# Optimization experiments

Hardware: AMD Instinct MI355X
Metric: run time of the kernel (lower is better)

Reference implementation:

```python
import jax, jax.numpy as jnp
import numpy as np

DIM = 1024
DIM_HEAD = 64
HEADS = 16
INNER = DIM_HEAD * HEADS  # 1024
B, N1, N2 = 8, 4096, 256
EPS = 1e-5


def layer_norm(x, w, b):
    mu = jnp.mean(x, axis=-1, keepdims=True)
    var = jnp.var(x, axis=-1, keepdims=True)
    return (x - mu) * jax.lax.rsqrt(var + EPS) * w + b


def setup_inputs() -> dict:
    key = jax.random.key(0)
    ks = jax.random.split(key, 10)
    return {
        "x": jax.random.normal(ks[0], (B, N1, DIM), jnp.float32),
        "latents": jax.random.normal(ks[1], (B, N2, DIM), jnp.float32),
        "shift": jax.random.normal(ks[2], (B, DIM), jnp.float32),
        "scale": jax.random.normal(ks[3], (B, DIM), jnp.float32),
        "ln1_w": jnp.ones((DIM,), jnp.float32),
        "ln1_b": jnp.zeros((DIM,), jnp.float32),
        "ln2_w": jnp.ones((DIM,), jnp.float32),
        "ln2_b": jnp.zeros((DIM,), jnp.float32),
        "Wq": jax.random.normal(ks[4], (INNER, DIM), jnp.float32) * 0.02,
        "Wkv": jax.random.normal(ks[5], (2 * INNER, DIM), jnp.float32) * 0.02,
        "Wo": jax.random.normal(ks[6], (DIM, INNER), jnp.float32) * 0.02,
    }


def reference(x, latents, shift, scale, ln1_w, ln1_b, ln2_w, ln2_b, Wq, Wkv, Wo):
    x = layer_norm(x, ln1_w, ln1_b)                      # (b, n1, D)
    lat = layer_norm(latents, ln2_w, ln2_b)              # (b, n2, D)
    lat = lat * (1.0 + scale[:, None, :]) + shift[:, None, :]

    b, n2, _ = lat.shape
    q = jnp.einsum('bld,ed->ble', lat, Wq)               # (b, n2, inner)
    kv_in = jnp.concatenate((x, lat), axis=-2)           # (b, n1+n2, D)
    kv = jnp.einsum('bld,ed->ble', kv_in, Wkv)           # (b, n1+n2, 2*inner)
    k, v = jnp.split(kv, 2, axis=-1)

    def to_heads(t):
        bsz, L, _ = t.shape
        return t.reshape(bsz, L, HEADS, DIM_HEAD).transpose(0, 2, 1, 3)

    q, k, v = to_heads(q), to_heads(k), to_heads(v)      # (b, h, L, dh)
    attn_scale = 1.0 / np.sqrt(np.sqrt(DIM_HEAD)).astype(np.float32)
    logits = jnp.einsum('bhqd,bhkd->bhqk', q * attn_scale, k * attn_scale)
    w = jax.nn.softmax(logits.astype(jnp.float32), axis=-1).astype(logits.dtype)
    out = jnp.einsum('bhqk,bhkd->bhqd', w, v)            # (b, h, n2, dh)
    out = out.transpose(0, 2, 1, 3).reshape(b, n2, INNER)
    return jnp.einsum('ble,de->bld', out, Wo)            # (b, n2, D)
```

## Files before the change

kernel.cpp:

```cpp
#include <hip/hip_runtime.h>
#include <cstdint>
#include <cstddef>

#define B_SZ 8
#define N1 4096
#define N2 256
#define LTOT 4352
#define DIMD 1024
#define HEADS 16
#define DH 64
#define MKV (B_SZ * LTOT)
#define ATILE 64
#define AITERS (LTOT / ATILE)
#define G0_BLOCKS 4352
#define MT_PER_XCD 34

typedef _Float16 f16;
typedef f16 f16x4_t __attribute__((ext_vector_type(4)));
typedef f16 f16x8_t __attribute__((ext_vector_type(8)));
typedef float f32x4_t __attribute__((ext_vector_type(4)));

__device__ __forceinline__ void g2l16(const void* g, void* l) {
  __builtin_amdgcn_global_load_lds(
      (__attribute__((address_space(1))) void*)g,
      (__attribute__((address_space(3))) void*)l, 16, 0, 0);
}


__global__ __launch_bounds__(256) void prep_kernel(
    const float* __restrict__ x, const float* __restrict__ lat,
    const float* __restrict__ shift, const float* __restrict__ scale,
    const float* __restrict__ ln1w, const float* __restrict__ ln1b,
    const float* __restrict__ ln2w, const float* __restrict__ ln2b,
    const float* __restrict__ Wq, const float* __restrict__ Wkv,
    const float* __restrict__ Wo, f16* __restrict__ kv_in,
    f16* __restrict__ Wq16, f16* __restrict__ Wkv16, f16* __restrict__ Wo16) {
  const int bid = blockIdx.x;
  const int tid = threadIdx.x;
  if (bid >= MKV) {
    const int c = bid - MKV;
    const float* src;
    f16* dst;
    int off;
    if (c < 1024) { src = Wq; dst = Wq16; off = c; }
    else if (c < 3072) { src = Wkv; dst = Wkv16; off = c - 1024; }
    else { src = Wo; dst = Wo16; off = c - 3072; }
    const int i = off * 256 + tid;
    float4 v = ((const float4*)src)[i];
    f16x4_t o = {(f16)v.x, (f16)v.y, (f16)v.z, (f16)v.w};
    ((f16x4_t*)dst)[i] = o;
    return;
  }
  const int row = bid;
  const int b = row / LTOT;
  const int n = row - b * LTOT;
  const bool is_lat = (n >= N1);
  const float* src = is_lat ? (lat + (size_t)(b * N2 + (n - N1)) * DIMD)
                            : (x + (size_t)(b * N1 + n) * DIMD);
  float4 v = ((const float4*)src)[tid];
  float s = v.x + v.y + v.z + v.w;
  float s2 = v.x * v.x + v.y * v.y + v.z * v.z + v.w * v.w;
#pragma unroll
  for (int m = 1; m <= 32; m <<= 1) {
    s += __shfl_xor(s, m, 64);
    s2 += __shfl_xor(s2, m, 64);
  }
  __shared__ float red[8];
  const int wave = tid >> 6;
  if ((tid & 63) == 0) { red[wave * 2] = s; red[wave * 2 + 1] = s2; }
  __syncthreads();
  s = red[0] + red[2] + red[4] + red[6];
  s2 = red[1] + red[3] + red[5] + red[7];
  const float mean = s * (1.0f / DIMD);
  const float var = fmaxf(s2 * (1.0f / DIMD) - mean * mean, 0.0f);
  const float rstd = rsqrtf(var + 1e-5f);
  const float4 w4 = ((const float4*)(is_lat ? ln2w : ln1w))[tid];
  const float4 b4 = ((const float4*)(is_lat ? ln2b : ln1b))[tid];
  float y0 = (v.x - mean) * rstd * w4.x + b4.x;
  float y1 = (v.y - mean) * rstd * w4.y + b4.y;
  float y2 = (v.z - mean) * rstd * w4.z + b4.z;
  float y3 = (v.w - mean) * rstd * w4.w + b4.w;
  if (is_lat) {
    float4 sc = ((const float4*)(scale + (size_t)b * DIMD))[tid];
    float4 sh = ((const float4*)(shift + (size_t)b * DIMD))[tid];
    y0 = y0 * (1.0f + sc.x) + sh.x;
    y1 = y1 * (1.0f + sc.y) + sh.y;
    y2 = y2 * (1.0f + sc.z) + sh.z;
    y3 = y3 * (1.0f + sc.w) + sh.w;
  }
  f16x4_t o = {(f16)y0, (f16)y1, (f16)y2, (f16)y3};
  *(f16x4_t*)(kv_in + (size_t)row * DIMD + tid * 4) = o;
}

__global__ __launch_bounds__(256, 4) void gemm_pre(
    const f16* __restrict__ kv_in, const f16* __restrict__ Wkv16,
    const f16* __restrict__ Wq16, f16* __restrict__ kbuf,
    f16* __restrict__ vbuf, f16* __restrict__ qbuf) {
  const int id = blockIdx.x;
  const bool is_kv = (id < G0_BLOCKS);
  int mt, nt;
  const f16 *Abase, *Bbase;
  if (is_kv) {
    const int xcd = id & 7, l = id >> 3;
    mt = xcd * MT_PER_XCD + (l >> 4);
    nt = l & 15;
    Abase = kv_in + (size_t)mt * 128 * DIMD;
    Bbase = Wkv16 + (size_t)nt * 128 * DIMD;
  } else {
    const int id2 = id - G0_BLOCKS;
    mt = id2 >> 3;
    nt = id2 & 7;
    const int bb = mt >> 1;
    Abase = kv_in + ((size_t)(bb * LTOT + N1 + (mt & 1) * 128)) * DIMD;
    Bbase = Wq16 + (size_t)nt * 128 * DIMD;
  }
  __shared__ alignas(16) f16 As[2][128 * 32];
  __shared__ alignas(16) f16 Bs[2][128 * 32];
  const int tid = threadIdx.x;
  const int wave = tid >> 6, lane = tid & 63;
  const int wm = (wave & 1) * 64, wn = (wave >> 1) * 64;
  const int lrow = lane >> 2, lcol = (lane & 3) * 8;
  const int r16 = lane & 15, g8 = (lane >> 4) * 8, q4 = (lane >> 4) * 4;
  const int lcol_sw = (((lane & 3) ^ ((lrow >> 1) & 3)) * 8);
  const int g8sw = (((lane >> 4) ^ ((r16 >> 1) & 3)) * 8);
  (void)lcol; (void)g8;
  f32x4_t acc[4][4] = {};

  auto stage = [&](int k0, int buf) {
    g2l16(Abase + (size_t)(wave * 16 + lrow) * DIMD + k0 + lcol_sw, &As[buf][(wave * 16) * 32]);
    g2l16(Abase + (size_t)(64 + wave * 16 + lrow) * DIMD + k0 + lcol_sw, &As[buf][(64 + wave * 16) * 32]);
    g2l16(Bbase + (size_t)(wave * 16 + lrow) * DIMD + k0 + lcol_sw, &Bs[buf][(wave * 16) * 32]);
    g2l16(Bbase + (size_t)(64 + wave * 16 + lrow) * DIMD + k0 + lcol_sw, &Bs[buf][(64 + wave * 16) * 32]);
  };
  auto body = [&](int kt, int cur) {
    if (kt < 31) asm volatile("s_waitcnt vmcnt(4)" ::: "memory");
    else         asm volatile("s_waitcnt vmcnt(0)" ::: "memory");
    asm volatile("s_barrier" ::: "memory");
    f16x8_t a[4], bf[4];
#pragma unroll
    for (int i = 0; i < 4; i++)
      a[i] = *(const f16x8_t*)&As[cur][(wm + i * 16 + r16) * 32 + g8sw];
#pragma unroll
    for (int j = 0; j < 4; j++)
      bf[j] = *(const f16x8_t*)&Bs[cur][(wn + j * 16 + r16) * 32 + g8sw];
#pragma unroll
    for (int i = 0; i < 4; i++)
#pragma unroll
      for (int j = 0; j < 4; j++)
        acc[i][j] = __builtin_amdgcn_mfma_f32_16x16x32_f16(a[i], bf[j], acc[i][j], 0, 0, 0);
    asm volatile("s_waitcnt lgkmcnt(0)" ::: "memory");
    asm volatile("s_barrier" ::: "memory");
    if (kt + 2 < 32) stage((kt + 2) * 32, cur);
  };
  stage(0, 0);
  stage(32, 1);
#pragma unroll 1
  for (int kt = 0; kt < 32; kt += 2) { body(kt, 0); body(kt + 1, 1); }

  if (is_kv) {
    const int m0 = mt * 128;
    const int b = m0 / LTOT;
    const int n0 = m0 - b * LTOT;
    const int e0 = nt * 128;
    if (e0 < 1024) {
#pragma unroll
      for (int i = 0; i < 4; i++) {
        const int n_base = n0 + wm + i * 16 + q4;
#pragma unroll
        for (int j = 0; j < 4; j++) {
          const int e = e0 + wn + j * 16 + r16;
          const int h = e >> 6, d = e & 63;
          const size_t base = ((size_t)(b * HEADS + h) * LTOT);
#pragma unroll
          for (int r = 0; r < 4; r++)
            kbuf[(base + n_base + r) * DH + d] = (f16)acc[i][j][r];
        }
      }
    } else {
      const int e0v = e0 - 1024;
#pragma unroll
      for (int i = 0; i < 4; i++) {
        const int n_base = n0 + wm + i * 16 + q4;
#pragma unroll
        for (int j = 0; j < 4; j++) {
          const int e = e0v + wn + j * 16 + r16;
          const int h = e >> 6, d = e & 63;
          f16x4_t pk = {(f16)acc[i][j][0], (f16)acc[i][j][1],
                        (f16)acc[i][j][2], (f16)acc[i][j][3]};
          *(f16x4_t*)&vbuf[((size_t)(b * HEADS + h) * DH + d) * LTOT + n_base] = pk;
        }
      }
    }
  } else {
    const int b = mt >> 1;
#pragma unroll
    for (int i = 0; i < 4; i++) {
      const int n_base = (mt & 1) * 128 + wm + i * 16 + q4;
#pragma unroll
      for (int j = 0; j < 4; j++) {
        const int e = nt * 128 + wn + j * 16 + r16;
        const int h = e >> 6, d = e & 63;
#pragma unroll
        for (int r = 0; r < 4; r++)
          qbuf[((size_t)(b * HEADS + h) * N2 + n_base + r) * DH + d] = (f16)acc[i][j][r];
      }
    }
  }
}

__global__ __launch_bounds__(256) void gemm_out(
    const f16* __restrict__ A0, const f16* __restrict__ BT,
    float* __restrict__ outp) {
  const int id = blockIdx.x;
  const int mt = id >> 4, nt = id & 15;
  const f16* Abase = A0 + (size_t)mt * 128 * DIMD;
  const f16* Bbase = BT + (size_t)nt * 64 * DIMD;
  __shared__ alignas(16) f16 As[2][128 * 32];
  __shared__ alignas(16) f16 Bs[2][64 * 32];
  const int tid = threadIdx.x;
  const int wave = tid >> 6, lane = tid & 63;
  const int wm = (wave & 1) * 64, wn = (wave >> 1) * 32;
  const int lrow = lane >> 2, lcol = (lane & 3) * 8;
  const int r16 = lane & 15, g8 = (lane >> 4) * 8, q4 = (lane >> 4) * 4;
  const int lcol_sw = (((lane & 3) ^ ((lrow >> 1) & 3)) * 8);
  const int g8sw = (((lane >> 4) ^ ((r16 >> 1) & 3)) * 8);
  (void)lcol; (void)g8;
  f32x4_t acc[4][2] = {};

  auto stage = [&](int k0, int buf) {
    g2l16(Abase + (size_t)(wave * 16 + lrow) * DIMD + k0 + lcol_sw, &As[buf][(wave * 16) * 32]);
    g2l16(Abase + (size_t)(64 + wave * 16 + lrow) * DIMD + k0 + lcol_sw, &As[buf][(64 + wave * 16) * 32]);
    g2l16(Bbase + (size_t)(wave * 16 + lrow) * DIMD + k0 + lcol_sw, &Bs[buf][(wave * 16) * 32]);
  };
  auto body = [&](int kt, int cur) {
    if (kt < 31) asm volatile("s_waitcnt vmcnt(3)" ::: "memory");
    else         asm volatile("s_waitcnt vmcnt(0)" ::: "memory");
    asm volatile("s_barrier" ::: "memory");
    f16x8_t a[4], bf[2];
#pragma unroll
    for (int i = 0; i < 4; i++)
      a[i] = *(const f16x8_t*)&As[cur][(wm + i * 16 + r16) * 32 + g8sw];
#pragma unroll
    for (int j = 0; j < 2; j++)
      bf[j] = *(const f16x8_t*)&Bs[cur][(wn + j * 16 + r16) * 32 + g8sw];
#pragma unroll
    for (int i = 0; i < 4; i++)
#pragma unroll
      for (int j = 0; j < 2; j++)
        acc[i][j] = __builtin_amdgcn_mfma_f32_16x16x32_f16(a[i], bf[j], acc[i][j], 0, 0, 0);
    asm volatile("s_waitcnt lgkmcnt(0)" ::: "memory");
    asm volatile("s_barrier" ::: "memory");
    if (kt + 2 < 32) stage((kt + 2) * 32, cur);
  };
  stage(0, 0);
  stage(32, 1);
#pragma unroll 1
  for (int kt = 0; kt < 32; kt += 2) { body(kt, 0); body(kt + 1, 1); }

  const int m0 = mt * 128, n0 = nt * 64;
#pragma unroll
  for (int i = 0; i < 4; i++) {
#pragma unroll
    for (int j = 0; j < 2; j++) {
      const int col = n0 + wn + j * 16 + r16;
#pragma unroll
      for (int r = 0; r < 4; r++)
        outp[(size_t)(m0 + wm + i * 16 + q4 + r) * DIMD + col] = acc[i][j][r];
    }
  }
}

__global__ __launch_bounds__(512, 2) void attn_kernel(
    const f16* __restrict__ qbuf, const f16* __restrict__ kbuf,
    const f16* __restrict__ vbuf, f16* __restrict__ attn_out) {
  const int bh = blockIdx.x & 127;
  const int qt = blockIdx.x >> 7;
  const int b = bh >> 4, h = bh & 15;
  const f16* qg = qbuf + ((size_t)bh * N2 + qt * 128) * DH;
  const f16* kg = kbuf + (size_t)bh * LTOT * DH;
  const f16* vg = vbuf + (size_t)bh * DH * LTOT;

  __shared__ alignas(16) f16 Ks[2][4096];
  __shared__ alignas(16) f16 Vs[2][4096];
  __shared__ alignas(16) f16 QP[9216];

  const int tid = threadIdx.x, wave = tid >> 6, lane = tid & 63;
  const int lrow = lane >> 2, lcol = (lane & 3) * 8;
  const int r16 = lane & 15, g8 = (lane >> 4) * 8, q4 = (lane >> 4) * 4;
  const int lcol_sw = (((lane & 3) ^ ((lrow >> 1) & 3)) * 8);
  const int g8sw = (((lane >> 4) ^ ((r16 >> 1) & 3)) * 8);
  (void)lcol;
  f16* Ps = &QP[wave * 1152];

#pragma unroll
  for (int i = 0; i < 2; i++) {
    const int c = wave * 2 + i, s = c >> 3, rb = (c & 7) * 16;
    g2l16(qg + (size_t)(rb + lrow) * DH + s * 32 + lcol_sw, &QP[s * 4096 + rb * 32]);
  }
  auto stage = [&](int kt, int buf) {
    const int s = wave >> 2, rb = (wave & 3) * 16;
    g2l16(kg + (size_t)(kt * ATILE + rb + lrow) * DH + s * 32 + lcol_sw,
          &Ks[buf][s * 2048 + rb * 32]);
    g2l16(vg + (size_t)(rb + lrow) * LTOT + kt * ATILE + s * 32 + lcol_sw,
          &Vs[buf][s * 2048 + rb * 32]);
  };
  stage(0, 0);
  stage(1, 1);
  asm volatile("s_waitcnt vmcnt(4)" ::: "memory");
  asm volatile("s_barrier" ::: "memory");
  f16x8_t bQ[2];
#pragma unroll
  for (int s = 0; s < 2; s++)
    bQ[s] = *(const f16x8_t*)&QP[s * 4096 + (wave * 16 + r16) * 32 + g8sw];
  asm volatile("s_waitcnt lgkmcnt(0)" ::: "memory");

  f32x4_t oacc[4] = {};
  float mrow = -1e30f, lsum = 0.0f;
  const float SCL = 0.125f * 1.44269504089f;

  for (int kt = 0; kt < AITERS; kt++) {
    const int cur = kt & 1;
    asm volatile("s_waitcnt vmcnt(2)" ::: "memory");
    asm volatile("s_barrier" ::: "memory");
    f32x4_t sacc[4] = {};
    __builtin_amdgcn_s_setprio(1);
#pragma unroll
    for (int s = 0; s < 2; s++) {
      f16x8_t aK[4];
#pragma unroll
      for (int i = 0; i < 4; i++)
        aK[i] = *(const f16x8_t*)&Ks[cur][s * 2048 + (i * 16 + r16) * 32 + g8sw];
#pragma unroll
      for (int i = 0; i < 4; i++)
        sacc[i] = __builtin_amdgcn_mfma_f32_16x16x32_f16(aK[i], bQ[s], sacc[i], 0, 0, 0);
    }
    __builtin_amdgcn_s_setprio(0);
    float vmax = -1e30f;
#pragma unroll
    for (int i = 0; i < 4; i++)
#pragma unroll
      for (int r = 0; r < 4; r++) vmax = fmaxf(vmax, sacc[i][r]);
    vmax = fmaxf(vmax, __shfl_xor(vmax, 16, 64));
    vmax = fmaxf(vmax, __shfl_xor(vmax, 32, 64));
    const float pm = SCL * vmax;
    if (!__all(pm <= mrow + 8.0f)) {
      const float m_new = fmaxf(mrow, pm);
      const float alpha = exp2f(mrow - m_new);
      lsum *= alpha;
#pragma unroll
      for (int id = 0; id < 4; id++) oacc[id] *= alpha;
      mrow = m_new;
    }
    float psum = 0.0f;
#pragma unroll
    for (int i = 0; i < 4; i++) {
      f16x4_t pk;
#pragma unroll
      for (int r = 0; r < 4; r++) {
        const float p = exp2f(SCL * sacc[i][r] - mrow);
        psum += p;
        pk[r] = (f16)p;
      }
      *(f16x4_t*)&Ps[r16 * 72 + i * 16 + q4] = pk;
    }
    psum += __shfl_xor(psum, 16, 64);
    psum += __shfl_xor(psum, 32, 64);
    lsum += psum;
    __builtin_amdgcn_s_setprio(1);
#pragma unroll
    for (int s2 = 0; s2 < 2; s2++) {
      f16x8_t aV[4];
#pragma unroll
      for (int id = 0; id < 4; id++)
        aV[id] = *(const f16x8_t*)&Vs[cur][s2 * 2048 + (id * 16 + r16) * 32 + g8sw];
      const f16x8_t bP = *(const f16x8_t*)&Ps[r16 * 72 + s2 * 32 + g8];
#pragma unroll
      for (int id = 0; id < 4; id++)
        oacc[id] = __builtin_amdgcn_mfma_f32_16x16x32_f16(aV[id], bP, oacc[id], 0, 0, 0);
    }
    __builtin_amdgcn_s_setprio(0);
    asm volatile("s_waitcnt lgkmcnt(0)" ::: "memory");
    asm volatile("s_barrier" ::: "memory");
    if (kt + 2 < AITERS) stage(kt + 2, cur);
  }
  const float inv = 1.0f / lsum;
  const int q = qt * 128 + wave * 16 + r16;
  const size_t rowbase = ((size_t)(b * N2 + q)) * DIMD + h * DH;
#pragma unroll
  for (int id = 0; id < 4; id++) {
    f16x4_t pk;
#pragma unroll
    for (int r = 0; r < 4; r++) pk[r] = (f16)(oacc[id][r] * inv);
    *(f16x4_t*)&attn_out[rowbase + id * 16 + q4] = pk;
  }
}

extern "C" void kernel_launch(void* const* d_in, const int* in_sizes, int n_in,
                              void* d_out, int out_size, void* d_ws, size_t ws_size,
                              hipStream_t stream) {
  const float* x     = (const float*)d_in[0];
  const float* lat   = (const float*)d_in[1];
  const float* shift = (const float*)d_in[2];
  const float* scale = (const float*)d_in[3];
  const float* ln1w  = (const float*)d_in[4];
  const float* ln1b  = (const float*)d_in[5];
  const float* ln2w  = (const float*)d_in[6];
  const float* ln2b  = (const float*)d_in[7];
  const float* Wq    = (const float*)d_in[8];
  const float* Wkv   = (const float*)d_in[9];
  const float* Wo    = (const float*)d_in[10];
  float* outp = (float*)d_out;

  char* ws = (char*)d_ws;
  f16* kv_in = (f16*)ws;                 ws += (size_t)MKV * DIMD * 2;
  f16* Wq16  = (f16*)ws;                 ws += (size_t)1024 * 1024 * 2;
  f16* Wkv16 = (f16*)ws;                 ws += (size_t)2048 * 1024 * 2;
  f16* Wo16  = (f16*)ws;                 ws += (size_t)1024 * 1024 * 2;
  f16* qbuf  = (f16*)ws;                 ws += (size_t)B_SZ * HEADS * N2 * DH * 2;
  f16* kbuf  = (f16*)ws;                 ws += (size_t)B_SZ * HEADS * LTOT * DH * 2;
  f16* vbuf  = (f16*)ws;                 ws += (size_t)B_SZ * HEADS * LTOT * DH * 2;
  f16* aout  = (f16*)ws;                 ws += (size_t)B_SZ * N2 * DIMD * 2;

  prep_kernel<<<dim3(MKV + 4096), dim3(256), 0, stream>>>(
      x, lat, shift, scale, ln1w, ln1b, ln2w, ln2b, Wq, Wkv, Wo,
      kv_in, Wq16, Wkv16, Wo16);
  gemm_pre<<<dim3(G0_BLOCKS + 128), dim3(256), 0, stream>>>(
      kv_in, Wkv16, Wq16, kbuf, vbuf, qbuf);
  attn_kernel<<<dim3(256), dim3(512), 0, stream>>>(qbuf, kbuf, vbuf, aout);
  gemm_out<<<dim3(256), dim3(256), 0, stream>>>(aout, Wo16, outp);
}
```

Measured before the change: 526.2 us.

## Enlarge QKV GEMM tiles to 256x256 with 8-wave ping-pong pipelined schedule

Measured after the change: 523.7 us. About the same (-0.5%).

```diff
diff --git a/kernel.cpp b/kernel.cpp
--- a/kernel.cpp
+++ b/kernel.cpp
@@ -12,8 +12,7 @@
 #define MKV (B_SZ * LTOT)
 #define ATILE 64
 #define AITERS (LTOT / ATILE)
-#define G0_BLOCKS 4352
-#define MT_PER_XCD 34
+#define G0B 1088
 
 typedef _Float16 f16;
 typedef f16 f16x4_t __attribute__((ext_vector_type(4)));
@@ -25,7 +24,6 @@
       (__attribute__((address_space(1))) void*)g,
       (__attribute__((address_space(3))) void*)l, 16, 0, 0);
 }
-
 
 __global__ __launch_bounds__(256) void prep_kernel(
     const float* __restrict__ x, const float* __restrict__ lat,
@@ -92,117 +90,164 @@
   *(f16x4_t*)(kv_in + (size_t)row * DIMD + tid * 4) = o;
 }
 
-__global__ __launch_bounds__(256, 4) void gemm_pre(
+#define DS_A(buf, mh)                                                          \
+  _Pragma("unroll") for (int i_ = 0; i_ < 4; i_++)                             \
+  _Pragma("unroll") for (int ks_ = 0; ks_ < 2; ks_++)                          \
+      aF[i_][ks_] = *(const f16x8_t*)&As[buf][mh][                             \
+          (wrow * 64 + i_ * 16 + r16) * 64 + (((ks_ * 4 + g8i) ^ xk) * 8)];
+
+#define DS_B(dst, buf, nh)                                                     \
+  _Pragma("unroll") for (int j_ = 0; j_ < 2; j_++)                             \
+  _Pragma("unroll") for (int ks_ = 0; ks_ < 2; ks_++)                          \
+      dst[j_][ks_] = *(const f16x8_t*)&Bs[buf][nh][                            \
+          (wcol * 32 + j_ * 16 + r16) * 64 + (((ks_ * 4 + g8i) ^ xk) * 8)];
+
+#define MFMA16(mh, nh, BF)                                                     \
+  __builtin_amdgcn_s_setprio(1);                                               \
+  _Pragma("unroll") for (int ks_ = 0; ks_ < 2; ks_++)                          \
+  _Pragma("unroll") for (int i_ = 0; i_ < 4; i_++)                             \
+  _Pragma("unroll") for (int j_ = 0; j_ < 2; j_++)                             \
+      acc[(mh)*4 + i_][(nh)*2 + j_] = __builtin_amdgcn_mfma_f32_16x16x32_f16(  \
+          aF[i_][ks_], BF[j_][ks_], acc[(mh)*4 + i_][(nh)*2 + j_], 0, 0, 0);   \
+  __builtin_amdgcn_s_setprio(0);
+
+#define BARR asm volatile("s_barrier" ::: "memory")
+#define LGKM0 asm volatile("s_waitcnt lgkmcnt(0)" ::: "memory")
+#define VM4 asm volatile("s_waitcnt vmcnt(4)" ::: "memory")
+
+__global__ __launch_bounds__(512, 2) void gemm_pre(
     const f16* __restrict__ kv_in, const f16* __restrict__ Wkv16,
     const f16* __restrict__ Wq16, f16* __restrict__ kbuf,
     f16* __restrict__ vbuf, f16* __restrict__ qbuf) {
   const int id = blockIdx.x;
-  const bool is_kv = (id < G0_BLOCKS);
-  int mt, nt;
+  const bool is_kv = (id < G0B);
+  int mt = 0, nt;
   const f16 *Abase, *Bbase;
   if (is_kv) {
     const int xcd = id & 7, l = id >> 3;
-    mt = xcd * MT_PER_XCD + (l >> 4);
-    nt = l & 15;
-    Abase = kv_in + (size_t)mt * 128 * DIMD;
-    Bbase = Wkv16 + (size_t)nt * 128 * DIMD;
+    mt = xcd * 17 + (l >> 3);
+    nt = l & 7;
+    Abase = kv_in + (size_t)mt * 256 * DIMD;
+    Bbase = Wkv16 + (size_t)nt * 256 * DIMD;
   } else {
-    const int id2 = id - G0_BLOCKS;
-    mt = id2 >> 3;
-    nt = id2 & 7;
-    const int bb = mt >> 1;
-    Abase = kv_in + ((size_t)(bb * LTOT + N1 + (mt & 1) * 128)) * DIMD;
-    Bbase = Wq16 + (size_t)nt * 128 * DIMD;
-  }
-  __shared__ alignas(16) f16 As[2][128 * 32];
-  __shared__ alignas(16) f16 Bs[2][128 * 32];
+    const int id2 = id - G0B;
+    const int bq = id2 >> 2;
+    nt = id2 & 3;
+    Abase = kv_in + ((size_t)(bq * LTOT + N1)) * DIMD;
+    Bbase = Wq16 + (size_t)nt * 256 * DIMD;
+  }
+  __shared__ alignas(16) f16 As[2][2][128 * 64];
+  __shared__ alignas(16) f16 Bs[2][2][128 * 64];
   const int tid = threadIdx.x;
   const int wave = tid >> 6, lane = tid & 63;
-  const int wm = (wave & 1) * 64, wn = (wave >> 1) * 64;
-  const int lrow = lane >> 2, lcol = (lane & 3) * 8;
-  const int r16 = lane & 15, g8 = (lane >> 4) * 8, q4 = (lane >> 4) * 4;
-  const int lcol_sw = (((lane & 3) ^ ((lrow >> 1) & 3)) * 8);
-  const int g8sw = (((lane >> 4) ^ ((r16 >> 1) & 3)) * 8);
-  (void)lcol; (void)g8;
-  f32x4_t acc[4][4] = {};
-
-  auto stage = [&](int k0, int buf) {
-    g2l16(Abase + (size_t)(wave * 16 + lrow) * DIMD + k0 + lcol_sw, &As[buf][(wave * 16) * 32]);
-    g2l16(Abase + (size_t)(64 + wave * 16 + lrow) * DIMD + k0 + lcol_sw, &As[buf][(64 + wave * 16) * 32]);
-    g2l16(Bbase + (size_t)(wave * 16 + lrow) * DIMD + k0 + lcol_sw, &Bs[buf][(wave * 16) * 32]);
-    g2l16(Bbase + (size_t)(64 + wave * 16 + lrow) * DIMD + k0 + lcol_sw, &Bs[buf][(64 + wave * 16) * 32]);
+  const int wrow = wave >> 2, wcol = wave & 3;
+  const int r16 = lane & 15, g8i = lane >> 4, q4 = (lane >> 4) * 4;
+  const int xk = r16 & 7;
+  const int t8 = tid >> 3, c8 = tid & 7;
+  f32x4_t acc[8][4] = {};
+  f16x8_t aF[4][2], b0F[2][2], b1F[2][2];
+
+  auto stageA = [&](int kt, int buf, int mh) {
+#pragma unroll
+    for (int j = 0; j < 2; j++) {
+      const int rih = j * 64 + t8;
+      const int row_g = j * 128 + mh * 64 + t8;
+      const int col8 = (c8 ^ (rih & 7)) * 8;
+      g2l16(Abase + (size_t)row_g * DIMD + kt * 64 + col8,
+            &As[buf][mh][(j * 512 + wave * 64) * 8]);
+    }
   };
-  auto body = [&](int kt, int cur) {
-    if (kt < 31) asm volatile("s_waitcnt vmcnt(4)" ::: "memory");
-    else         asm volatile("s_waitcnt vmcnt(0)" ::: "memory");
-    asm volatile("s_barrier" ::: "memory");
-    f16x8_t a[4], bf[4];
-#pragma unroll
-    for (int i = 0; i < 4; i++)
-      a[i] = *(const f16x8_t*)&As[cur][(wm + i * 16 + r16) * 32 + g8sw];
-#pragma unroll
-    for (int j = 0; j < 4; j++)
-      bf[j] = *(const f16x8_t*)&Bs[cur][(wn + j * 16 + r16) * 32 + g8sw];
-#pragma unroll
-    for (int i = 0; i < 4; i++)
-#pragma unroll
-      for (int j = 0; j < 4; j++)
-        acc[i][j] = __builtin_amdgcn_mfma_f32_16x16x32_f16(a[i], bf[j], acc[i][j], 0, 0, 0);
-    asm volatile("s_waitcnt lgkmcnt(0)" ::: "memory");
-    asm volatile("s_barrier" ::: "memory");
-    if (kt + 2 < 32) stage((kt + 2) * 32, cur);
+  auto stageB = [&](int kt, int buf, int nh) {
+#pragma unroll
+    for (int j = 0; j < 2; j++) {
+      const int rih = j * 64 + t8;
+      const int row_g = (rih >> 5) * 64 + nh * 32 + (rih & 31);
+      const int col8 = (c8 ^ (rih & 7)) * 8;
+      g2l16(Bbase + (size_t)row_g * DIMD + kt * 64 + col8,
+            &Bs[buf][nh][(j * 512 + wave * 64) * 8]);
+    }
   };
-  stage(0, 0);
-  stage(32, 1);
+
+  stageA(0, 0, 0); stageB(0, 0, 1); stageA(0, 0, 1); stageB(0, 0, 0);
+  stageA(1, 1, 0); stageB(1, 1, 1);
+  VM4; BARR;
+
 #pragma unroll 1
-  for (int kt = 0; kt < 32; kt += 2) { body(kt, 0); body(kt + 1, 1); }
+  for (int it = 0; it < 8; ++it) {
+    const int kA = 2 * it + 1;
+    const int kB = (2 * it + 2 > 15) ? 15 : 2 * it + 2;
+    const int kC = (2 * it + 3 > 15) ? 15 : 2 * it + 3;
+    DS_A(0, 0); DS_B(b0F, 0, 0);
+    stageA(kA, 1, 1);
+    BARR; LGKM0; MFMA16(0, 0, b0F); BARR;
+    DS_B(b1F, 0, 1);
+    stageB(kA, 1, 0);
+    BARR; LGKM0; MFMA16(0, 1, b1F); BARR;
+    DS_A(0, 1);
+    stageA(kB, 0, 0);
+    BARR; LGKM0; MFMA16(1, 1, b1F); BARR;
+    stageB(kB, 0, 1);
+    VM4;
+    BARR; LGKM0; MFMA16(1, 0, b0F); BARR;
+    DS_A(1, 0); DS_B(b0F, 1, 0);
+    stageA(kB, 0, 1);
+    BARR; LGKM0; MFMA16(0, 0, b0F); BARR;
+    DS_B(b1F, 1, 1);
+    stageB(kB, 0, 0);
+    BARR; LGKM0; MFMA16(0, 1, b1F); BARR;
+    DS_A(1, 1);
+    stageA(kC, 1, 0);
+    BARR; LGKM0; MFMA16(1, 1, b1F); BARR;
+    stageB(kC, 1, 1);
+    VM4;
+    BARR; LGKM0; MFMA16(1, 0, b0F); BARR;
+  }
+  asm volatile("s_waitcnt vmcnt(0)" ::: "memory");
 
   if (is_kv) {
-    const int m0 = mt * 128;
+    const int m0 = mt * 256;
     const int b = m0 / LTOT;
     const int n0 = m0 - b * LTOT;
-    const int e0 = nt * 128;
-    if (e0 < 1024) {
-#pragma unroll
-      for (int i = 0; i < 4; i++) {
-        const int n_base = n0 + wm + i * 16 + q4;
-#pragma unroll
-        for (int j = 0; j < 4; j++) {
-          const int e = e0 + wn + j * 16 + r16;
+    if (nt < 4) {
+#pragma unroll
+      for (int ai = 0; ai < 8; ai++) {
+        const int n_base = n0 + wrow * 128 + (ai >> 2) * 64 + (ai & 3) * 16 + q4;
+#pragma unroll
+        for (int bj = 0; bj < 4; bj++) {
+          const int e = nt * 256 + wcol * 64 + (bj >> 1) * 32 + (bj & 1) * 16 + r16;
           const int h = e >> 6, d = e & 63;
-          const size_t base = ((size_t)(b * HEADS + h) * LTOT);
+          const size_t base = (size_t)(b * HEADS + h) * LTOT;
 #pragma unroll
           for (int r = 0; r < 4; r++)
-            kbuf[(base + n_base + r) * DH + d] = (f16)acc[i][j][r];
+            kbuf[(base + n_base + r) * DH + d] = (f16)acc[ai][bj][r];
         }
       }
     } else {
-      const int e0v = e0 - 1024;
-#pragma unroll
-      for (int i = 0; i < 4; i++) {
-        const int n_base = n0 + wm + i * 16 + q4;
-#pragma unroll
-        for (int j = 0; j < 4; j++) {
-          const int e = e0v + wn + j * 16 + r16;
+#pragma unroll
+      for (int ai = 0; ai < 8; ai++) {
+        const int n_base = n0 + wrow * 128 + (ai >> 2) * 64 + (ai & 3) * 16 + q4;
+#pragma unroll
+        for (int bj = 0; bj < 4; bj++) {
+          const int e = (nt - 4) * 256 + wcol * 64 + (bj >> 1) * 32 + (bj & 1) * 16 + r16;
           const int h = e >> 6, d = e & 63;
-          f16x4_t pk = {(f16)acc[i][j][0], (f16)acc[i][j][1],
-                        (f16)acc[i][j][2], (f16)acc[i][j][3]};
+          f16x4_t pk = {(f16)acc[ai][bj][0], (f16)acc[ai][bj][1],
+                        (f16)acc[ai][bj][2], (f16)acc[ai][bj][3]};
           *(f16x4_t*)&vbuf[((size_t)(b * HEADS + h) * DH + d) * LTOT + n_base] = pk;
         }
       }
     }
   } else {
-    const int b = mt >> 1;
-#pragma unroll
-    for (int i = 0; i < 4; i++) {
-      const int n_base = (mt & 1) * 128 + wm + i * 16 + q4;
-#pragma unroll
-      for (int j = 0; j < 4; j++) {
-        const int e = nt * 128 + wn + j * 16 + r16;
+    const int b = (id - G0B) >> 2;
+#pragma unroll
+    for (int ai = 0; ai < 8; ai++) {
+      const int qn = wrow * 128 + (ai >> 2) * 64 + (ai & 3) * 16 + q4;
+#pragma unroll
+      for (int bj = 0; bj < 4; bj++) {
+        const int e = nt * 256 + wcol * 64 + (bj >> 1) * 32 + (bj & 1) * 16 + r16;
         const int h = e >> 6, d = e & 63;
 #pragma unroll
         for (int r = 0; r < 4; r++)
-          qbuf[((size_t)(b * HEADS + h) * N2 + n_base + r) * DH + d] = (f16)acc[i][j][r];
+          qbuf[((size_t)(b * HEADS + h) * N2 + qn + r) * DH + d] = (f16)acc[ai][bj][r];
       }
     }
   }
@@ -220,11 +265,10 @@
   const int tid = threadIdx.x;
   const int wave = tid >> 6, lane = tid & 63;
   const int wm = (wave & 1) * 64, wn = (wave >> 1) * 32;
-  const int lrow = lane >> 2, lcol = (lane & 3) * 8;
-  const int r16 = lane & 15, g8 = (lane >> 4) * 8, q4 = (lane >> 4) * 4;
+  const int lrow = lane >> 2;
+  const int r16 = lane & 15, q4 = (lane >> 4) * 4;
   const int lcol_sw = (((lane & 3) ^ ((lrow >> 1) & 3)) * 8);
   const int g8sw = (((lane >> 4) ^ ((r16 >> 1) & 3)) * 8);
-  (void)lcol; (void)g8;
   f32x4_t acc[4][2] = {};
 
   auto stage = [&](int k0, int buf) {
@@ -285,11 +329,10 @@
   __shared__ alignas(16) f16 QP[9216];
 
   const int tid = threadIdx.x, wave = tid >> 6, lane = tid & 63;
-  const int lrow = lane >> 2, lcol = (lane & 3) * 8;
+  const int lrow = lane >> 2;
   const int r16 = lane & 15, g8 = (lane >> 4) * 8, q4 = (lane >> 4) * 4;
   const int lcol_sw = (((lane & 3) ^ ((lrow >> 1) & 3)) * 8);
   const int g8sw = (((lane >> 4) ^ ((r16 >> 1) & 3)) * 8);
-  (void)lcol;
   f16* Ps = &QP[wave * 1152];
 
 #pragma unroll
@@ -424,7 +467,7 @@
   prep_kernel<<<dim3(MKV + 4096), dim3(256), 0, stream>>>(
       x, lat, shift, scale, ln1w, ln1b, ln2w, ln2b, Wq, Wkv, Wo,
       kv_in, Wq16, Wkv16, Wo16);
-  gemm_pre<<<dim3(G0_BLOCKS + 128), dim3(256), 0, stream>>>(
+  gemm_pre<<<dim3(G0B + 32), dim3(512), 0, stream>>>(
       kv_in, Wkv16, Wq16, kbuf, vbuf, qbuf);
   attn_kernel<<<dim3(256), dim3(512), 0, stream>>>(qbuf, kbuf, vbuf, aout);
   gemm_out<<<dim3(256), dim3(256), 0, stream>>>(aout, Wo16, outp);
```
